# Optimization experiments

Measured on AMD Instinct MI355X. Metric: run time of the kernel, lower is better.

Reference implementation:

```python
import jax, jax.numpy as jnp
import numpy as np

N = 50000   # nodes
E = 800000  # edges
IN, H1, H2, OUT = 128, 256, 128, 1


def setup_inputs() -> dict:
    key = jax.random.key(0)
    ks = jax.random.split(key, 9)
    x = jax.random.normal(ks[0], (N, IN), dtype=jnp.float32)
    edge_index = jax.random.randint(ks[1], (2, E), 0, N, dtype=jnp.int32)
    def glorot(k, fan_in, fan_out):
        s = np.sqrt(6.0 / (fan_in + fan_out)).astype(np.float32)
        return jax.random.uniform(k, (fan_in, fan_out), jnp.float32, -s, s)
    W1 = glorot(ks[2], IN, H1)
    b1 = jnp.zeros((H1,), jnp.float32)
    W2 = glorot(ks[3], H1, H2)
    b2 = jnp.zeros((H2,), jnp.float32)
    W3 = glorot(ks[4], H2, OUT)
    b3 = jnp.zeros((OUT,), jnp.float32)
    return {"x": x, "edge_index": edge_index, "W1": W1, "b1": b1,
            "W2": W2, "b2": b2, "W3": W3, "b3": b3}


def _gcn_layer(x, W, b, src, dst, norm):
    # dense transform [N, d_in] @ [d_in, d_out]
    h = x @ W
    # degree-normalized sparse aggregation: out[dst] += norm * h[src]
    agg = jax.ops.segment_sum(h[src] * norm[:, None], dst, num_segments=N)
    return agg + b


def reference(x, edge_index, W1, b1, W2, b2, W3, b3):
    src, dst = edge_index[0], edge_index[1]
    # PyG GCNConv: add self loops, then symmetric normalization
    loop = jnp.arange(N, dtype=src.dtype)
    src = jnp.concatenate([src, loop])
    dst = jnp.concatenate([dst, loop])
    deg = jax.ops.segment_sum(jnp.ones_like(dst, jnp.float32), dst, num_segments=N)
    dis = jax.lax.rsqrt(jnp.maximum(deg, 1.0))  # deg >= 1 via self loops
    norm = dis[src] * dis[dst]  # [E+N]
    h1 = jax.nn.relu(_gcn_layer(x, W1, b1, src, dst, norm))
    h2 = jax.nn.relu(_gcn_layer(h1, W2, b2, src, dst, norm))
    y = _gcn_layer(h2, W3, b3, src, dst, norm).reshape(-1)
    return (y, h1, h2)
```

## Files before the change

### kernel.cpp

```cpp
#include <hip/hip_runtime.h>


typedef __attribute__((ext_vector_type(8))) short short8;
typedef __attribute__((ext_vector_type(4))) float f32x4;

static __device__ __forceinline__ unsigned short f2bf(float f){
  union { float f; unsigned u; } v; v.f = f;
  unsigned r = v.u + 0x7FFF + ((v.u >> 16) & 1);
  return (unsigned short)(r >> 16);
}
static __device__ __forceinline__ float2 bf2f2(unsigned u){
  union { unsigned u; float f; } a, b;
  a.u = u << 16; b.u = u & 0xffff0000u;
  return make_float2(a.f, b.f);
}

__global__ __launch_bounds__(256) void k_prepbin(
    const int* __restrict__ src, const int* __restrict__ dst,
    int* __restrict__ bcur, unsigned* __restrict__ pairs, int E, int binB,
    const float* __restrict__ W1, const float* __restrict__ W2,
    unsigned short* __restrict__ Wf1, unsigned short* __restrict__ Wf2){
  __shared__ int cl[256];
  int blk = blockIdx.x;
  int tid = threadIdx.x;
  if (blk < binB){
    int e0 = blk * 4096 + tid;
    cl[tid] = 0; __syncthreads();
    #pragma unroll
    for (int i = 0; i < 16; i++){
      int e = e0 + i*256;
      if (e < E) atomicAdd(&cl[dst[e] >> 8], 1);
    }
    __syncthreads();
    int c = cl[tid];
    int g = (c > 0) ? atomicAdd(&bcur[tid], c) : 0;
    cl[tid] = g;
    __syncthreads();
    #pragma unroll
    for (int i = 0; i < 16; i++){
      int e = e0 + i*256;
      if (e < E){
        int d = dst[e];
        int b = d >> 8;
        int p = atomicAdd(&cl[b], 1);
        pairs[(b << 13) + p] = (unsigned)src[e] | ((unsigned)(d & 255) << 16);
      }
    }
  } else {
    int t = (blk - binB)*256 + tid;
    if (t < 32768){
      int j = t & 7, lane = (t>>3) & 63, kt = (t>>9) & 3, nt = t >> 11;
      int nn = nt*16 + (lane & 15);
      int kk = kt*32 + (lane>>4)*8 + j;
      Wf1[t] = f2bf(W1[kk*256 + nn]);
    } else {
      int o = t - 32768;
      int j = o & 7, lane = (o>>3) & 63, ntl = (o>>9) & 3, kt = (o>>11) & 7, h = o >> 14;
      int nn = (h*4 + ntl)*16 + (lane & 15);
      int kk = kt*32 + (lane>>4)*8 + j;
      Wf2[o] = f2bf(W2[kk*128 + nn]);
    }
  }
}

__global__ __launch_bounds__(256) void k_place(
    const int* __restrict__ bcur, const unsigned* __restrict__ pairs,
    unsigned short* __restrict__ csr_src, int* __restrict__ rowptr,
    int* __restrict__ cnt, float* __restrict__ dis,
    const float4* __restrict__ x, uint2* __restrict__ xbs,
    int n, int nb){
  __shared__ int sh[256];
  __shared__ int ncnt[256];
  __shared__ float disl[256];
  int t = threadIdx.x;
  int b = blockIdx.x;
  int v = (t < nb) ? bcur[t] : 0;
  sh[t] = v; __syncthreads();
  for (int off = 1; off < 256; off <<= 1){
    int xx = (t >= off) ? sh[t-off] : 0;
    __syncthreads(); sh[t] += xx; __syncthreads();
  }
  int csr_base = (b == 0) ? 0 : sh[b-1];
  int cnt_b = bcur[b];
  ncnt[t] = 0; __syncthreads();
  const unsigned* P = pairs + ((size_t)b << 13);
  for (int i = t; i < cnt_b; i += 256) atomicAdd(&ncnt[P[i] >> 16], 1);
  __syncthreads();
  int c = ncnt[t];
  sh[t] = c; __syncthreads();
  for (int off = 1; off < 256; off <<= 1){
    int xx = (t >= off) ? sh[t-off] : 0;
    __syncthreads(); sh[t] += xx; __syncthreads();
  }
  int noff = sh[t] - c;
  int node = (b << 8) + t;
  float di = rsqrtf((float)(c + 1));
  disl[t] = di;
  if (node < n){
    rowptr[node] = csr_base + noff;
    cnt[node] = c;
    dis[node] = di;
  }
  ncnt[t] = noff; __syncthreads();
  for (int i = t; i < cnt_b; i += 256){
    unsigned u = P[i];
    int p = atomicAdd(&ncnt[u >> 16], 1);
    csr_src[csr_base + p] = (unsigned short)(u & 0xffff);
  }
  const float4* xg = x + (size_t)b*8192;
  uint2* xo = xbs + (size_t)b*8192;
  int lim = n*32 - b*8192;
  for (int i = t; i < 8192 && i < lim; i += 256){
    float d = disl[i >> 5];
    float4 vv = xg[i];
    xo[i] = make_uint2((unsigned)f2bf(d*vv.x) | ((unsigned)f2bf(d*vv.y) << 16),
                       (unsigned)f2bf(d*vv.z) | ((unsigned)f2bf(d*vv.w) << 16));
  }
}

__global__ void k_aggL1(const unsigned* __restrict__ xbs, unsigned* __restrict__ out,
                        const int* __restrict__ rowptr, const int* __restrict__ cnt,
                        const unsigned short* __restrict__ csr_src,
                        const float* __restrict__ dis, int n){
  int t = threadIdx.x;
  int lane = t & 63;
  int node = blockIdx.x*4 + (t >> 6);
  if (node >= n) return;
  float di = dis[node];
  float2 acc = bf2f2(xbs[(size_t)node*64 + lane]);
  int start = rowptr[node];
  int mm = cnt[node];
  int j = 0;
  for (; j + 15 < mm; j += 16){
    int s[16]; unsigned uv[16];
    #pragma unroll
    for (int q = 0; q < 16; q++) s[q] = csr_src[start+j+q];
    #pragma unroll
    for (int q = 0; q < 16; q++) uv[q] = xbs[(size_t)s[q]*64 + lane];
    #pragma unroll
    for (int q = 0; q < 16; q++){
      float2 u = bf2f2(uv[q]);
      acc.x += u.x; acc.y += u.y;
    }
  }
  for (; j + 3 < mm; j += 4){
    int s[4]; unsigned uv[4];
    #pragma unroll
    for (int q = 0; q < 4; q++) s[q] = csr_src[start+j+q];
    #pragma unroll
    for (int q = 0; q < 4; q++) uv[q] = xbs[(size_t)s[q]*64 + lane];
    #pragma unroll
    for (int q = 0; q < 4; q++){
      float2 u = bf2f2(uv[q]);
      acc.x += u.x; acc.y += u.y;
    }
  }
  for (; j < mm; j++){
    float2 u = bf2f2(xbs[(size_t)csr_src[start+j]*64 + lane]);
    acc.x += u.x; acc.y += u.y;
  }
  out[(size_t)node*64 + lane] =
      (unsigned)f2bf(di*acc.x) | ((unsigned)f2bf(di*acc.y) << 16);
}

__global__ __launch_bounds__(512) void k_gemm12(
    const unsigned short* __restrict__ Xa,
    const unsigned short* __restrict__ Wf1, const unsigned short* __restrict__ Wf2,
    const float* __restrict__ b1, const float* __restrict__ dis,
    float* __restrict__ h1, unsigned short* __restrict__ T2s, int n)
{
  __shared__ unsigned short h1l[64*256];
  int t = threadIdx.x;
  int w = t >> 6, lane = t & 63, m = lane & 15, q = lane >> 4;
  int row0 = blockIdx.x * 64;
  int stripe = w & 3;
  int nth = w >> 2;
  int rowm = row0 + stripe*16 + m;
  int ra = (rowm < n) ? rowm : (n-1);

  short8 af[4];
  {
    const short8* Arow = (const short8*)(Xa + (size_t)ra*128);
    #pragma unroll
    for (int kt = 0; kt < 4; kt++) af[kt] = Arow[kt*4 + q];
  }
  f32x4 acc1[8];
  #pragma unroll
  for (int i = 0; i < 8; i++) acc1[i] = (f32x4){0.f,0.f,0.f,0.f};
  const short8* Wv1 = (const short8*)Wf1;
  #pragma unroll
  for (int nt = 0; nt < 8; nt++){
    int ntg = nth*8 + nt;
    #pragma unroll
    for (int kt = 0; kt < 4; kt++){
      short8 bfr = Wv1[(ntg*4 + kt)*64 + lane];
      acc1[nt] = __builtin_amdgcn_mfma_f32_16x16x32_bf16(af[kt], bfr, acc1[nt], 0, 0, 0);
    }
  }
  int rowa = row0 + stripe*16 + q*4;
  int rla  = stripe*16 + q*4;
  #pragma unroll
  for (int nt = 0; nt < 8; nt++){
    int col = nth*128 + nt*16 + m;
    float b = b1[col];
    #pragma unroll
    for (int r = 0; r < 4; r++){
      int rr = rowa + r;
      float o = fmaxf(acc1[nt][r] + b, 0.0f);
      if (rr < n) h1[(size_t)rr*256 + col] = o;
      int rl = rla + r;
      unsigned byte = (unsigned)(rl*512) + (((unsigned)col*2) ^ ((unsigned)(rl & 7) << 4));
      *(unsigned short*)((char*)h1l + byte) = f2bf(o);
    }
  }
  __syncthreads();

  short8 af2[8];
  {
    int rl = stripe*16 + m;
    #pragma unroll
    for (int kt = 0; kt < 8; kt++){
      unsigned byte = (unsigned)(rl*512) + (((unsigned)(kt*64 + q*16)) ^ ((unsigned)(rl & 7) << 4));
      af2[kt] = *(const short8*)((const char*)h1l + byte);
    }
  }
  f32x4 acc2[4];
  #pragma unroll
  for (int i = 0; i < 4; i++) acc2[i] = (f32x4){0.f,0.f,0.f,0.f};
  const short8* Wv2 = (const short8*)Wf2;
  #pragma unroll
  for (int nt = 0; nt < 4; nt++){
    #pragma unroll
    for (int kt = 0; kt < 8; kt++){
      short8 bfr = Wv2[((nth*8 + kt)*4 + nt)*64 + lane];
      acc2[nt] = __builtin_amdgcn_mfma_f32_16x16x32_bf16(af2[kt], bfr, acc2[nt], 0, 0, 0);
    }
  }
  float dsv[4];
  #pragma unroll
  for (int r = 0; r < 4; r++){
    int rr = rowa + r;
    dsv[r] = (rr < n) ? dis[rr] : 0.0f;
  }
  #pragma unroll
  for (int nt = 0; nt < 4; nt++){
    int col = nth*64 + nt*16 + m;
    #pragma unroll
    for (int r = 0; r < 4; r++){
      int rr = rowa + r;
      if (rr < n) T2s[(size_t)rr*128 + col] = f2bf(dsv[r] * acc2[nt][r]);
    }
  }
}

__global__ void k_aggL2(const unsigned* __restrict__ t2s, float* __restrict__ h2,
                        const int* __restrict__ rowptr, const int* __restrict__ cnt,
                        const unsigned short* __restrict__ csr_src,
                        const float* __restrict__ dis,
                        const float* __restrict__ b2, const float* __restrict__ W3,
                        float* __restrict__ u, int n){
  int t = threadIdx.x;
  int lane = t & 63;
  int node = blockIdx.x*4 + (t >> 6);
  if (node >= n) return;
  float di = dis[node];
  float2 acc = bf2f2(t2s[(size_t)node*64 + lane]);
  int start = rowptr[node];
  int mm = cnt[node];
  int j = 0;
  for (; j + 15 < mm; j += 16){
    int s[16]; unsigned uv[16];
    #pragma unroll
    for (int q = 0; q < 16; q++) s[q] = csr_src[start+j+q];
    #pragma unroll
    for (int q = 0; q < 16; q++) uv[q] = t2s[(size_t)s[q]*64 + lane];
    #pragma unroll
    for (int q = 0; q < 16; q++){
      float2 uu = bf2f2(uv[q]);
      acc.x += uu.x; acc.y += uu.y;
    }
  }
  for (; j + 3 < mm; j += 4){
    int s[4]; unsigned uv[4];
    #pragma unroll
    for (int q = 0; q < 4; q++) s[q] = csr_src[start+j+q];
    #pragma unroll
    for (int q = 0; q < 4; q++) uv[q] = t2s[(size_t)s[q]*64 + lane];
    #pragma unroll
    for (int q = 0; q < 4; q++){
      float2 uu = bf2f2(uv[q]);
      acc.x += uu.x; acc.y += uu.y;
    }
  }
  for (; j < mm; j++){
    float2 uu = bf2f2(t2s[(size_t)csr_src[start+j]*64 + lane]);
    acc.x += uu.x; acc.y += uu.y;
  }
  float2 b = ((const float2*)b2)[lane];
  acc.x = fmaxf(fmaf(di, acc.x, b.x), 0.0f);
  acc.y = fmaxf(fmaf(di, acc.y, b.y), 0.0f);
  ((float2*)h2)[(size_t)node*64 + lane] = acc;
  float up = fmaf(acc.x, W3[2*lane], acc.y * W3[2*lane+1]);
  #pragma unroll
  for (int off = 32; off > 0; off >>= 1) up += __shfl_down(up, off);
  if (lane == 0) u[node] = di * up;
}

__global__ void k_agg1d(const float* __restrict__ us, float* __restrict__ y,
                        const int* __restrict__ rowptr, const int* __restrict__ cnt,
                        const unsigned short* __restrict__ csr_src,
                        const float* __restrict__ dis,
                        const float* __restrict__ b3, int n){
  int t = threadIdx.x;
  int node = blockIdx.x*16 + (t >> 4);
  int sub = t & 15;
  if (node >= n) return;
  int s0 = rowptr[node];
  int m = cnt[node];
  float acc = (sub == 0) ? us[node] : 0.0f;
  for (int j = sub; j < m; j += 16)
    acc += us[csr_src[s0 + j]];
  #pragma unroll
  for (int off = 8; off > 0; off >>= 1) acc += __shfl_xor(acc, off);
  if (sub == 0) y[node] = fmaf(dis[node], acc, b3[0]);
}

extern "C" void kernel_launch(void* const* d_in, const int* in_sizes, int n_in,
                              void* d_out, int out_size, void* d_ws, size_t ws_size,
                              hipStream_t stream){
  const float* x  = (const float*)d_in[0];
  const int*  ei  = (const int*)d_in[1];
  const float* W1 = (const float*)d_in[2];
  const float* b1 = (const float*)d_in[3];
  const float* W2 = (const float*)d_in[4];
  const float* b2 = (const float*)d_in[5];
  const float* W3 = (const float*)d_in[6];
  const float* b3 = (const float*)d_in[7];
  const int N = in_sizes[0] / 128;
  const int E = in_sizes[1] / 2;
  const int* src = ei;
  const int* dst = ei + E;
  const int NB = (N + 255) >> 8;

  char* p = (char*)d_ws;
  auto alloc = [&](size_t bytes)->char*{
    char* r = p; p += (bytes + 255) & ~(size_t)255; return r;
  };
  int*   bcur    = (int*)  alloc(256*4);
  int*   rowptr  = (int*)  alloc((size_t)N*4);
  int*   cnt     = (int*)  alloc((size_t)N*4);
  float* dis     = (float*)alloc((size_t)N*4);
  unsigned* pairs = (unsigned*)alloc((size_t)NB*8192*4);
  unsigned short* csr_src = (unsigned short*)alloc((size_t)E*2);
  unsigned* xbs  = (unsigned*)alloc((size_t)N*128*2);
  unsigned* xa   = (unsigned*)alloc((size_t)N*128*2);
  unsigned short* t2s = (unsigned short*)alloc((size_t)N*128*2);
  float* u       = (float*)alloc((size_t)N*4);
  unsigned short* wf1 = (unsigned short*)alloc(32768*2);
  unsigned short* wf2 = (unsigned short*)alloc(32768*2);

  float* y  = (float*)d_out;
  float* h1 = y + N;
  float* h2 = h1 + (size_t)N*256;

  int bb = (E + 4095)/4096;

  hipMemsetAsync(bcur, 0, 256*4, stream);
  k_prepbin <<<bb + 256, 256, 0, stream>>>(
      src, dst, bcur, pairs, E, bb, W1, W2, wf1, wf2);
  k_place   <<<NB, 256, 0, stream>>>(bcur, pairs, csr_src, rowptr, cnt, dis,
                                     (const float4*)x, (uint2*)xbs, N, NB);

  int ab = (N + 3)/4;
  int rb = (N + 63)/64;
  k_aggL1   <<<ab, 256, 0, stream>>>(xbs, (unsigned*)xa, rowptr, cnt, csr_src, dis, N);
  k_gemm12  <<<rb, 512, 0, stream>>>((const unsigned short*)xa, wf1, wf2, b1, dis,
                                     h1, t2s, N);
  k_aggL2   <<<ab, 256, 0, stream>>>((const unsigned*)t2s, h2, rowptr, cnt,
                                     csr_src, dis, b2, W3, u, N);
  k_agg1d   <<<(N + 15)/16, 256, 0, stream>>>(u, y, rowptr, cnt, csr_src, dis, b3, N);
}
```

Measured before the change: 242.8 us.

## Build CSR with global-atomic count, block scan and scatter instead of binning

The CSR construction no longer buckets edges into per-256-node bins in LDS and then places them. It now runs three kernels. The first counts in-degrees with global atomics and also converts the weights. The second takes a per-block prefix scan, with the block base taken from a global cursor atomic, and fuses the x scaling. The third scatters source indices using per-node global atomic cursors. This removes the intermediate pairs buffer and its second pass, in exchange for contended global atomics, an extra launch and a larger memset. Neighbour order within a row becomes nondeterministic, which can change float summation order.

```diff
diff --git a/kernel.cpp b/kernel.cpp
--- a/kernel.cpp
+++ b/kernel.cpp
@@ -15,39 +15,21 @@
   return make_float2(a.f, b.f);
 }
 
-__global__ __launch_bounds__(256) void k_prepbin(
-    const int* __restrict__ src, const int* __restrict__ dst,
-    int* __restrict__ bcur, unsigned* __restrict__ pairs, int E, int binB,
+__global__ __launch_bounds__(256) void k_count(
+    const int* __restrict__ dst, int* __restrict__ cnt, int E, int cb,
     const float* __restrict__ W1, const float* __restrict__ W2,
     unsigned short* __restrict__ Wf1, unsigned short* __restrict__ Wf2){
-  __shared__ int cl[256];
   int blk = blockIdx.x;
   int tid = threadIdx.x;
-  if (blk < binB){
+  if (blk < cb){
     int e0 = blk * 4096 + tid;
-    cl[tid] = 0; __syncthreads();
     #pragma unroll
     for (int i = 0; i < 16; i++){
       int e = e0 + i*256;
-      if (e < E) atomicAdd(&cl[dst[e] >> 8], 1);
-    }
-    __syncthreads();
-    int c = cl[tid];
-    int g = (c > 0) ? atomicAdd(&bcur[tid], c) : 0;
-    cl[tid] = g;
-    __syncthreads();
-    #pragma unroll
-    for (int i = 0; i < 16; i++){
-      int e = e0 + i*256;
-      if (e < E){
-        int d = dst[e];
-        int b = d >> 8;
-        int p = atomicAdd(&cl[b], 1);
-        pairs[(b << 13) + p] = (unsigned)src[e] | ((unsigned)(d & 255) << 16);
-      }
+      if (e < E) atomicAdd(&cnt[dst[e]], 1);
     }
   } else {
-    int t = (blk - binB)*256 + tid;
+    int t = (blk - cb)*256 + tid;
     if (t < 32768){
       int j = t & 7, lane = (t>>3) & 63, kt = (t>>9) & 3, nt = t >> 11;
       int nn = nt*16 + (lane & 15);
@@ -63,49 +45,32 @@
   }
 }
 
-__global__ __launch_bounds__(256) void k_place(
-    const int* __restrict__ bcur, const unsigned* __restrict__ pairs,
-    unsigned short* __restrict__ csr_src, int* __restrict__ rowptr,
-    int* __restrict__ cnt, float* __restrict__ dis,
-    const float4* __restrict__ x, uint2* __restrict__ xbs,
-    int n, int nb){
+__global__ __launch_bounds__(256) void k_scanx(
+    const int* __restrict__ cnt, int* __restrict__ rowptr, int* __restrict__ cur,
+    float* __restrict__ dis, int* __restrict__ cursor,
+    const float4* __restrict__ x, uint2* __restrict__ xbs, int n){
   __shared__ int sh[256];
-  __shared__ int ncnt[256];
   __shared__ float disl[256];
+  __shared__ int sbase;
   int t = threadIdx.x;
   int b = blockIdx.x;
-  int v = (t < nb) ? bcur[t] : 0;
-  sh[t] = v; __syncthreads();
-  for (int off = 1; off < 256; off <<= 1){
-    int xx = (t >= off) ? sh[t-off] : 0;
-    __syncthreads(); sh[t] += xx; __syncthreads();
-  }
-  int csr_base = (b == 0) ? 0 : sh[b-1];
-  int cnt_b = bcur[b];
-  ncnt[t] = 0; __syncthreads();
-  const unsigned* P = pairs + ((size_t)b << 13);
-  for (int i = t; i < cnt_b; i += 256) atomicAdd(&ncnt[P[i] >> 16], 1);
-  __syncthreads();
-  int c = ncnt[t];
+  int node = b*256 + t;
+  int c = (node < n) ? cnt[node] : 0;
+  float di = rsqrtf((float)(c + 1));
+  disl[t] = di;
   sh[t] = c; __syncthreads();
   for (int off = 1; off < 256; off <<= 1){
     int xx = (t >= off) ? sh[t-off] : 0;
     __syncthreads(); sh[t] += xx; __syncthreads();
   }
   int noff = sh[t] - c;
-  int node = (b << 8) + t;
-  float di = rsqrtf((float)(c + 1));
-  disl[t] = di;
+  if (t == 255) sbase = atomicAdd(cursor, sh[255]);
+  __syncthreads();
+  int base = sbase;
   if (node < n){
-    rowptr[node] = csr_base + noff;
-    cnt[node] = c;
-    dis[node] = di;
-  }
-  ncnt[t] = noff; __syncthreads();
-  for (int i = t; i < cnt_b; i += 256){
-    unsigned u = P[i];
-    int p = atomicAdd(&ncnt[u >> 16], 1);
-    csr_src[csr_base + p] = (unsigned short)(u & 0xffff);
+    rowptr[node] = base + noff;
+    cur[node]    = base + noff;
+    dis[node]    = di;
   }
   const float4* xg = x + (size_t)b*8192;
   uint2* xo = xbs + (size_t)b*8192;
@@ -115,6 +80,17 @@
     float4 vv = xg[i];
     xo[i] = make_uint2((unsigned)f2bf(d*vv.x) | ((unsigned)f2bf(d*vv.y) << 16),
                        (unsigned)f2bf(d*vv.z) | ((unsigned)f2bf(d*vv.w) << 16));
+  }
+}
+
+__global__ __launch_bounds__(256) void k_scatter(
+    const int* __restrict__ src, const int* __restrict__ dst,
+    int* __restrict__ cur, unsigned short* __restrict__ csr_src, int E){
+  int e = blockIdx.x*256 + threadIdx.x;
+  if (e < E){
+    int d = dst[e];
+    int p = atomicAdd(&cur[d], 1);
+    csr_src[p] = (unsigned short)src[e];
   }
 }
 
@@ -346,11 +322,11 @@
   auto alloc = [&](size_t bytes)->char*{
     char* r = p; p += (bytes + 255) & ~(size_t)255; return r;
   };
-  int*   bcur    = (int*)  alloc(256*4);
   int*   rowptr  = (int*)  alloc((size_t)N*4);
   int*   cnt     = (int*)  alloc((size_t)N*4);
+  int*   cur     = (int*)  alloc((size_t)N*4);
+  int*   cursor  = (int*)  alloc(256);
   float* dis     = (float*)alloc((size_t)N*4);
-  unsigned* pairs = (unsigned*)alloc((size_t)NB*8192*4);
   unsigned short* csr_src = (unsigned short*)alloc((size_t)E*2);
   unsigned* xbs  = (unsigned*)alloc((size_t)N*128*2);
   unsigned* xa   = (unsigned*)alloc((size_t)N*128*2);
@@ -363,13 +339,14 @@
   float* h1 = y + N;
   float* h2 = h1 + (size_t)N*256;
 
-  int bb = (E + 4095)/4096;
-
-  hipMemsetAsync(bcur, 0, 256*4, stream);
-  k_prepbin <<<bb + 256, 256, 0, stream>>>(
-      src, dst, bcur, pairs, E, bb, W1, W2, wf1, wf2);
-  k_place   <<<NB, 256, 0, stream>>>(bcur, pairs, csr_src, rowptr, cnt, dis,
-                                     (const float4*)x, (uint2*)xbs, N, NB);
+  int cb = (E + 4095)/4096;
+
+  hipMemsetAsync(cnt, 0, (size_t)N*4, stream);
+  hipMemsetAsync(cursor, 0, 4, stream);
+  k_count   <<<cb + 256, 256, 0, stream>>>(dst, cnt, E, cb, W1, W2, wf1, wf2);
+  k_scanx   <<<NB, 256, 0, stream>>>(cnt, rowptr, cur, dis, cursor,
+                                     (const float4*)x, (uint2*)xbs, N);
+  k_scatter <<<(E + 255)/256, 256, 0, stream>>>(src, dst, cur, csr_src, E);
 
   int ab = (N + 3)/4;
   int rb = (N + 63)/64;
```

Result: slower. 299.4 us (+23.3%).
